# Kernel tuning notes

Measured on AMD Instinct MI355X. Metric: run time of the kernel, lower is better.

The kernel has to match this reference:

```python
import jax, jax.numpy as jnp
import numpy as np

E = 8          # num_experts
TOP_K = 2      # router top-k
ALPHA = 1.702  # swigluoai alpha
LIMIT = 7.0    # swigluoai clamp limit


def setup_inputs() -> dict:
    key = jax.random.key(0)
    ks = jax.random.split(key, 7)
    B, S, H, I = 2, 1024, 1024, 1024
    s = 1.0 / np.sqrt(H)  # keep activations O(1), realistic init scale
    return {
        "x": jax.random.normal(ks[0], (B, S, H), jnp.float32),
        "router_weight": jax.random.normal(ks[1], (E, H), jnp.float32) * s,
        "router_bias": jax.random.normal(ks[2], (E,), jnp.float32) * 0.01,
        "w1": jax.random.normal(ks[3], (E, H, 2 * I), jnp.float32) * s,  # interleaved gate/up
        "w1_bias": jax.random.normal(ks[4], (E, 2 * I), jnp.float32) * 0.01,
        "w2": jax.random.normal(ks[5], (E, I, H), jnp.float32) * s,
        "w2_bias": jax.random.normal(ks[6], (E, H), jnp.float32) * 0.01,
    }


def _moe(x, router_weight, router_bias, w1, w1_bias, w2, w2_bias):
    B, S, H = x.shape
    xf = x.reshape(-1, H)                                   # [T, H]
    # ---- router: softmax over expert logits, then top-k ----
    logits = xf @ router_weight.T + router_bias             # [T, E]
    probs = jax.nn.softmax(logits, axis=-1)
    expert_weights, expert_ids = jax.lax.top_k(probs, TOP_K)  # [T, k]
    # combine weights scattered to dense [T, E] (no normalization: normalize_expert_weights=None)
    combine = jnp.sum(jax.nn.one_hot(expert_ids, E, dtype=xf.dtype)
                      * expert_weights[..., None], axis=1)  # [T, E]
    # ---- grouped MLP, expressed densely per expert (reference semantics) ----
    h = jnp.einsum('th,ehi->eti', xf, w1) + w1_bias[:, None, :]   # [E, T, 2I]
    gate = h[..., 0::2]                                          # interleaved layout
    up = h[..., 1::2]
    gate = jnp.minimum(gate, LIMIT)                              # swigluoai: clamp gate max
    up = jnp.clip(up, -LIMIT, LIMIT)                             # clamp up both sides
    glu = gate * jax.nn.sigmoid(gate * ALPHA)
    act = (up + 1.0) * glu                                       # [E, T, I]
    y = jnp.einsum('eti,eih->eth', act, w2) + w2_bias[:, None, :]  # [E, T, H]
    out = jnp.einsum('eth,te->th', y, combine)                   # weighted combine
    return out.reshape(B, S, H), expert_weights


def reference(x, router_weight, router_bias, w1, w1_bias, w2, w2_bias):
    return _moe(x, router_weight, router_bias, w1, w1_bias, w2, w2_bias)
```

## Files before the change

### kernel.cpp

```cpp
#include <hip/hip_runtime.h>
#include <cstdint>
#include <cstddef>

typedef unsigned short u16;
typedef short bf16x8 __attribute__((ext_vector_type(8)));
typedef float floatx4 __attribute__((ext_vector_type(4)));

#define GLD16(gp, sp) __builtin_amdgcn_global_load_lds(                      \
    (const __attribute__((address_space(1))) void*)(gp),                     \
    (__attribute__((address_space(3))) void*)(sp), 16, 0, 0)

#define VWAIT(N) asm volatile("s_waitcnt vmcnt(" #N ")" ::: "memory")
#define BARF()                                                               \
  do {                                                                       \
    __builtin_amdgcn_sched_barrier(0);                                       \
    __builtin_amdgcn_s_barrier();                                            \
    __builtin_amdgcn_sched_barrier(0);                                       \
  } while (0)

__device__ __forceinline__ u16 f2bf(float f) {
  unsigned u = __float_as_uint(f);
  u += 0x7fffu + ((u >> 16) & 1u);
  return (u16)(u >> 16);
}

__device__ __forceinline__ void transpose64(const float* __restrict__ inb, u16* __restrict__ outb,
                                            int C, int r0, int c0) {
  __shared__ float tileT[64][65];
  const int t = threadIdx.x;
  const int k = t & 15, w = t >> 4;
#pragma unroll
  for (int it = 0; it < 4; ++it) {
    const int r = r0 + w + it * 16;
    const float4 v = *(const float4*)(inb + (size_t)r * C + (c0 + k * 4));
    tileT[k * 4 + 0][w + it * 16] = v.x;
    tileT[k * 4 + 1][w + it * 16] = v.y;
    tileT[k * 4 + 2][w + it * 16] = v.z;
    tileT[k * 4 + 3][w + it * 16] = v.w;
  }
  __syncthreads();
#pragma unroll
  for (int it = 0; it < 4; ++it) {
    const int cc = w + it * 16;
    const int r4 = k * 4;
    ushort4 o;
    o.x = f2bf(tileT[cc][r4 + 0]);
    o.y = f2bf(tileT[cc][r4 + 1]);
    o.z = f2bf(tileT[cc][r4 + 2]);
    o.w = f2bf(tileT[cc][r4 + 3]);
    *(ushort4*)(outb + (size_t)(c0 + cc) * 1024 + r0 + r4) = o;
  }
}

__global__ __launch_bounds__(256) void front_kernel(
    const float* __restrict__ x, const float* __restrict__ rw, const float* __restrict__ rb,
    float* __restrict__ ew, int* __restrict__ eids, float* __restrict__ eprobs,
    u16* __restrict__ xb,
    const float* __restrict__ w1, u16* __restrict__ w1t,
    const float* __restrict__ w2, u16* __restrict__ w2t) {
  const int bid = blockIdx.x;
  if (bid >= 512) {
    int idx = bid - 512;
    if (idx < 4096) {
      const int e = idx >> 9, rem = idx & 511;
      const int ct = rem & 31, rt = rem >> 5;
      transpose64(w1 + (size_t)e * 1024 * 2048, w1t + (size_t)e * 2048 * 1024,
                  2048, rt * 64, ct * 64);
    } else {
      idx -= 4096;
      const int e = idx >> 8, rem = idx & 255;
      const int ct = rem & 15, rt = rem >> 4;
      transpose64(w2 + (size_t)e * 1024 * 1024, w2t + (size_t)e * 1024 * 1024,
                  1024, rt * 64, ct * 64);
    }
    return;
  }
  const int wave = threadIdx.x >> 6, lane = threadIdx.x & 63;
  const int t = bid * 4 + wave;
  const float4* xv = (const float4*)(x + (size_t)t * 1024);
  ushort4* xo = (ushort4*)(xb + (size_t)t * 1024);
  float acc[8];
#pragma unroll
  for (int e = 0; e < 8; ++e) acc[e] = 0.f;
  for (int j = lane; j < 256; j += 64) {
    float4 xx = xv[j];
    ushort4 o;
    o.x = f2bf(xx.x); o.y = f2bf(xx.y); o.z = f2bf(xx.z); o.w = f2bf(xx.w);
    xo[j] = o;
#pragma unroll
    for (int e = 0; e < 8; ++e) {
      float4 wv = ((const float4*)(rw + (size_t)e * 1024))[j];
      acc[e] += xx.x * wv.x + xx.y * wv.y + xx.z * wv.z + xx.w * wv.w;
    }
  }
#pragma unroll
  for (int e = 0; e < 8; ++e) {
    float v = acc[e];
#pragma unroll
    for (int off = 32; off > 0; off >>= 1) v += __shfl_down(v, off);
    acc[e] = v;
  }
  if (lane == 0) {
    float p[8];
    float mx = -1e30f;
#pragma unroll
    for (int e = 0; e < 8; ++e) { p[e] = acc[e] + rb[e]; mx = fmaxf(mx, p[e]); }
    float sum = 0.f;
#pragma unroll
    for (int e = 0; e < 8; ++e) { p[e] = __expf(p[e] - mx); sum += p[e]; }
    float inv = 1.f / sum;
#pragma unroll
    for (int e = 0; e < 8; ++e) p[e] *= inv;
    int i0 = 0;
#pragma unroll
    for (int e = 1; e < 8; ++e) if (p[e] > p[i0]) i0 = e;
    int i1 = (i0 == 0) ? 1 : 0;
#pragma unroll
    for (int e = 0; e < 8; ++e) if (e != i0 && e != i1 && p[e] > p[i1]) i1 = e;
    ew[t * 2 + 0] = p[i0];
    ew[t * 2 + 1] = p[i1];
    eids[t * 2 + 0] = i0;
    eids[t * 2 + 1] = i1;
    eprobs[t * 2 + 0] = p[i0];
    eprobs[t * 2 + 1] = p[i1];
  }
}

__global__ void build_lists_kernel(const int* __restrict__ eids, const float* __restrict__ eprobs,
                                   int* __restrict__ row_token, float* __restrict__ row_scale,
                                   int* __restrict__ tok2slot, int* __restrict__ meta) {
  __shared__ int cnt[8], base[8], cur[8];
  const int tid = threadIdx.x;
  if (tid < 8) { cnt[tid] = 0; cur[tid] = 0; }
  __syncthreads();
  for (int t = tid; t < 2048; t += 256) {
    atomicAdd(&cnt[eids[t * 2 + 0]], 1);
    atomicAdd(&cnt[eids[t * 2 + 1]], 1);
  }
  __syncthreads();
  if (tid == 0) {
    int off = 0, w = 0;
    for (int e = 0; e < 8; ++e) {
      base[e] = off;
      meta[48 + e] = off;
      int nb = (cnt[e] + 127) >> 7;
      for (int rb = 0; rb < nb; ++rb) meta[1 + w++] = (e << 8) | rb;
      off += nb << 7;
    }
    meta[0] = w;
  }
  __syncthreads();
  for (int s = tid; s < 5120; s += 256) { row_token[s] = -1; row_scale[s] = 0.f; }
  __syncthreads();
  for (int t = tid; t < 2048; t += 256) {
#pragma unroll
    for (int k = 0; k < 2; ++k) {
      int e = eids[t * 2 + k];
      int s = base[e] + atomicAdd(&cur[e], 1);
      row_token[s] = t;
      row_scale[s] = eprobs[t * 2 + k];
      tok2slot[t * 2 + k] = s;
    }
  }
}

__device__ __forceinline__ void g1_compute(const u16* AsR, const u16* BsR, int wr, int wc,
                                           int lane, floatx4 (&acc)[4][4]) {
  bf16x8 af[4], bfr[4];
#pragma unroll
  for (int mi = 0; mi < 4; ++mi) af[mi] = *(const bf16x8*)(AsR + (wr * 4 + mi) * 512 + lane * 8);
#pragma unroll
  for (int ni = 0; ni < 4; ++ni) bfr[ni] = *(const bf16x8*)(BsR + (wc * 4 + ni) * 512 + lane * 8);
  __builtin_amdgcn_s_setprio(1);
#pragma unroll
  for (int mi = 0; mi < 4; ++mi)
#pragma unroll
    for (int ni = 0; ni < 4; ++ni)
      acc[mi][ni] = __builtin_amdgcn_mfma_f32_16x16x32_bf16(af[mi], bfr[ni], acc[mi][ni], 0, 0, 0);
  __builtin_amdgcn_s_setprio(0);
}

__global__ __launch_bounds__(256) void gemm1_act_kernel(
    const u16* __restrict__ xb, const u16* __restrict__ w1t,
    const float* __restrict__ w1b,
    const int* __restrict__ row_token, const float* __restrict__ row_scale,
    const int* __restrict__ meta, u16* __restrict__ actS) {
  if ((int)blockIdx.x >= meta[0]) return;
  __shared__ __align__(16) u16 As[3][128 * 32];
  __shared__ __align__(16) u16 Bs[3][128 * 32];
  const int w = meta[1 + blockIdx.x];
  const int e = w >> 8, rb = w & 255;
  const int slotB = meta[48 + e] + rb * 128;
  const int colBase = blockIdx.y * 128;
  const int tid = threadIdx.x, lane = tid & 63, wave = tid >> 6;
  const int row16 = lane & 15, chunk = lane >> 4;
  const u16* Bt = w1t + (size_t)e * 2048 * 1024;
  const u16* aP[2]; const u16* bP[2];
#pragma unroll
  for (int r = 0; r < 2; ++r) {
    int g = r * 4 + wave;
    int tk = row_token[slotB + g * 16 + row16];
    if (tk < 0) tk = 0;
    aP[r] = xb + (size_t)tk * 1024 + chunk * 8;
    bP[r] = Bt + (size_t)(colBase + g * 16 + row16) * 1024 + chunk * 8;
  }
  const int wr = wave >> 1, wc = wave & 1;
  floatx4 acc[4][4];
#pragma unroll
  for (int mi = 0; mi < 4; ++mi)
#pragma unroll
    for (int ni = 0; ni < 4; ++ni) acc[mi][ni] = floatx4{0.f, 0.f, 0.f, 0.f};

#define G1_STAGE(W, KT)                                                      \
  {                                                                          \
    const int kk = (KT) * 32;                                                \
    GLD16(aP[0] + kk, As[W] + wave * 512);                                   \
    GLD16(bP[0] + kk, Bs[W] + wave * 512);                                   \
    GLD16(aP[1] + kk, As[W] + (4 + wave) * 512);                             \
    GLD16(bP[1] + kk, Bs[W] + (4 + wave) * 512);                             \
  }

  G1_STAGE(0, 0);
  G1_STAGE(1, 1);

#pragma unroll 1
  for (int kt = 0; kt < 30; kt += 3) {
    G1_STAGE(2, kt + 2); VWAIT(8); BARF();
    g1_compute(As[0], Bs[0], wr, wc, lane, acc); BARF();
    G1_STAGE(0, kt + 3); VWAIT(8); BARF();
    g1_compute(As[1], Bs[1], wr, wc, lane, acc); BARF();
    G1_STAGE(1, kt + 4); VWAIT(8); BARF();
    g1_compute(As[2], Bs[2], wr, wc, lane, acc); BARF();
  }
  VWAIT(4); BARF();
  g1_compute(As[0], Bs[0], wr, wc, lane, acc); BARF();
  VWAIT(0); BARF();
  g1_compute(As[1], Bs[1], wr, wc, lane, acc);
#undef G1_STAGE

  const int cl = lane & 15, ql = lane >> 4;
#pragma unroll
  for (int mi = 0; mi < 4; ++mi) {
#pragma unroll
    for (int r = 0; r < 4; ++r) {
      const int slot = slotB + wr * 64 + mi * 16 + ql * 4 + r;
      const float c = row_scale[slot];
#pragma unroll
      for (int ni = 0; ni < 4; ++ni) {
        const int n = colBase + wc * 64 + ni * 16 + cl;
        float v = acc[mi][ni][r] + w1b[e * 2048 + n];
        float o = __shfl_xor(v, 1);
        if ((lane & 1) == 0) {
          float g = fminf(v, 7.f);
          float u = fminf(fmaxf(o, -7.f), 7.f);
          float sg = 1.f / (1.f + __expf(-1.702f * g));
          float a = (u + 1.f) * (g * sg);
          actS[(size_t)slot * 1024 + (n >> 1)] = f2bf(c * a);
        }
      }
    }
  }
}

__global__ __launch_bounds__(256) void gemm2_kernel(
    const u16* __restrict__ actS, const u16* __restrict__ w2t,
    const int* __restrict__ meta, float* __restrict__ y) {
  if ((int)blockIdx.x >= meta[0]) return;
  __shared__ __align__(16) u16 As[3][128 * 32];
  __shared__ __align__(16) u16 Bs[3][128 * 32];
  const int w = meta[1 + blockIdx.x];
  const int e = w >> 8, rb = w & 255;
  const int slotB = meta[48 + e] + rb * 128;
  const int colBase = blockIdx.y * 128;
  const int tid = threadIdx.x, lane = tid & 63, wave = tid >> 6;
  const int row16 = lane & 15, chunk = lane >> 4;
  const u16* Bt = w2t + (size_t)e * 1024 * 1024;
  const u16* aP[2]; const u16* bP[2];
#pragma unroll
  for (int r = 0; r < 2; ++r) {
    int g = r * 4 + wave;
    aP[r] = actS + (size_t)(slotB + g * 16 + row16) * 1024 + chunk * 8;
    bP[r] = Bt + (size_t)(colBase + g * 16 + row16) * 1024 + chunk * 8;
  }
  const int wr = wave >> 1, wc = wave & 1;
  floatx4 acc[4][4];
#pragma unroll
  for (int mi = 0; mi < 4; ++mi)
#pragma unroll
    for (int ni = 0; ni < 4; ++ni) acc[mi][ni] = floatx4{0.f, 0.f, 0.f, 0.f};

#define G2_STAGE(W, KT)                                                      \
  {                                                                          \
    const int kk = (KT) * 32;                                                \
    GLD16(aP[0] + kk, As[W] + wave * 512);                                   \
    GLD16(bP[0] + kk, Bs[W] + wave * 512);                                   \
    GLD16(aP[1] + kk, As[W] + (4 + wave) * 512);                             \
    GLD16(bP[1] + kk, Bs[W] + (4 + wave) * 512);                             \
  }

  G2_STAGE(0, 0);
  G2_STAGE(1, 1);

#pragma unroll 1
  for (int kt = 0; kt < 30; kt += 3) {
    G2_STAGE(2, kt + 2); VWAIT(8); BARF();
    g1_compute(As[0], Bs[0], wr, wc, lane, acc); BARF();
    G2_STAGE(0, kt + 3); VWAIT(8); BARF();
    g1_compute(As[1], Bs[1], wr, wc, lane, acc); BARF();
    G2_STAGE(1, kt + 4); VWAIT(8); BARF();
    g1_compute(As[2], Bs[2], wr, wc, lane, acc); BARF();
  }
  VWAIT(4); BARF();
  g1_compute(As[0], Bs[0], wr, wc, lane, acc); BARF();
  VWAIT(0); BARF();
  g1_compute(As[1], Bs[1], wr, wc, lane, acc);
#undef G2_STAGE

  const int cl = lane & 15, ql = lane >> 4;
#pragma unroll
  for (int mi = 0; mi < 4; ++mi)
#pragma unroll
    for (int r = 0; r < 4; ++r) {
      const int slot = slotB + wr * 64 + mi * 16 + ql * 4 + r;
#pragma unroll
      for (int ni = 0; ni < 4; ++ni) {
        const int col = colBase + wc * 64 + ni * 16 + cl;
        y[(size_t)slot * 1024 + col] = acc[mi][ni][r];
      }
    }
}

__global__ void combine_kernel(const float* __restrict__ y, const int* __restrict__ eids,
                               const float* __restrict__ eprobs, const int* __restrict__ tok2slot,
                               const float* __restrict__ w2b, float* __restrict__ out) {
  int idx = blockIdx.x * 256 + threadIdx.x;
  int t = idx >> 10, h = idx & 1023;
  int e0 = eids[t * 2], e1 = eids[t * 2 + 1];
  int s0 = tok2slot[t * 2], s1 = tok2slot[t * 2 + 1];
  out[idx] = eprobs[t * 2] * w2b[e0 * 1024 + h] + eprobs[t * 2 + 1] * w2b[e1 * 1024 + h]
           + y[(size_t)s0 * 1024 + h] + y[(size_t)s1 * 1024 + h];
}

extern "C" void kernel_launch(void* const* d_in, const int* in_sizes, int n_in,
                              void* d_out, int out_size, void* d_ws, size_t ws_size,
                              hipStream_t stream) {
  const float* x   = (const float*)d_in[0];
  const float* rw  = (const float*)d_in[1];
  const float* rb  = (const float*)d_in[2];
  const float* w1  = (const float*)d_in[3];
  const float* w1b = (const float*)d_in[4];
  const float* w2  = (const float*)d_in[5];
  const float* w2b = (const float*)d_in[6];
  float* out = (float*)d_out;
  float* ew  = out + (size_t)2048 * 1024;

  char* ws = (char*)d_ws;
  u16* xb        = (u16*)(ws);
  u16* w1t       = (u16*)(ws + (4ull << 20));
  float* y       = (float*)(ws + (4ull << 20));
  u16* w2t       = (u16*)(ws + (36ull << 20));
  u16* actS      = (u16*)(ws + (52ull << 20));
  int* eids      = (int*)(ws + (62ull << 20));
  float* eprobs  = (float*)(ws + (62ull << 20) + (16 << 10));
  int* row_token = (int*)(ws + (62ull << 20) + (32 << 10));
  float* row_scale = (float*)(ws + (62ull << 20) + (52 << 10));
  int* meta      = (int*)(ws + (62ull << 20) + (72 << 10));
  int* tok2slot  = (int*)(ws + (62ull << 20) + (74 << 10));

  front_kernel<<<512 + 4096 + 2048, 256, 0, stream>>>(x, rw, rb, ew, eids, eprobs, xb,
                                                      w1, w1t, w2, w2t);
  build_lists_kernel<<<1, 256, 0, stream>>>(eids, eprobs, row_token, row_scale, tok2slot, meta);
  gemm1_act_kernel<<<dim3(40, 16), 256, 0, stream>>>(xb, w1t, w1b, row_token, row_scale, meta, actS);
  gemm2_kernel<<<dim3(40, 8), 256, 0, stream>>>(actS, w2t, meta, y);
  combine_kernel<<<8192, 256, 0, stream>>>(y, eids, eprobs, tok2slot, w2b, out);
}
```

Before: 250.5 us.

## Fuse combine into gemm2 via atomic scatter-add and init output in gemm1

Removes the separate combine kernel and the intermediate y buffer. gemm1 blocks now also write the bias-weighted initial output (probability-weighted w2 bias), and gemm2 atomically adds its scaled results straight into the token rows of the output. This avoids writing and re-reading a 5120x1024 fp32 buffer and saves one launch. In exchange it adds float atomics, whose summation order is nondeterministic, and relies on gemm1 finishing before gemm2 on the same stream.

```diff
diff --git a/kernel.cpp b/kernel.cpp
--- a/kernel.cpp
+++ b/kernel.cpp
@@ -128,7 +128,7 @@
 
 __global__ void build_lists_kernel(const int* __restrict__ eids, const float* __restrict__ eprobs,
                                    int* __restrict__ row_token, float* __restrict__ row_scale,
-                                   int* __restrict__ tok2slot, int* __restrict__ meta) {
+                                   int* __restrict__ meta) {
   __shared__ int cnt[8], base[8], cur[8];
   const int tid = threadIdx.x;
   if (tid < 8) { cnt[tid] = 0; cur[tid] = 0; }
@@ -159,7 +159,6 @@
       int s = base[e] + atomicAdd(&cur[e], 1);
       row_token[s] = t;
       row_scale[s] = eprobs[t * 2 + k];
-      tok2slot[t * 2 + k] = s;
     }
   }
 }
@@ -184,7 +183,28 @@
     const u16* __restrict__ xb, const u16* __restrict__ w1t,
     const float* __restrict__ w1b,
     const int* __restrict__ row_token, const float* __restrict__ row_scale,
-    const int* __restrict__ meta, u16* __restrict__ actS) {
+    const int* __restrict__ meta, u16* __restrict__ actS,
+    const int* __restrict__ eids, const float* __restrict__ eprobs,
+    const float* __restrict__ w2b, float* __restrict__ out) {
+  const int tid = threadIdx.x;
+  {
+    const int gtid = (blockIdx.y * gridDim.x + blockIdx.x) * 256 + tid;
+    const float4* b4 = (const float4*)w2b;
+    float4* o4 = (float4*)out;
+    for (int i = gtid; i < 524288; i += 640 * 256) {
+      const int t = i >> 8, h4 = i & 255;
+      const int e0 = eids[t * 2], e1 = eids[t * 2 + 1];
+      const float p0 = eprobs[t * 2], p1 = eprobs[t * 2 + 1];
+      const float4 b0 = b4[e0 * 256 + h4];
+      const float4 b1 = b4[e1 * 256 + h4];
+      float4 r;
+      r.x = p0 * b0.x + p1 * b1.x;
+      r.y = p0 * b0.y + p1 * b1.y;
+      r.z = p0 * b0.z + p1 * b1.z;
+      r.w = p0 * b0.w + p1 * b1.w;
+      o4[i] = r;
+    }
+  }
   if ((int)blockIdx.x >= meta[0]) return;
   __shared__ __align__(16) u16 As[3][128 * 32];
   __shared__ __align__(16) u16 Bs[3][128 * 32];
@@ -192,7 +212,7 @@
   const int e = w >> 8, rb = w & 255;
   const int slotB = meta[48 + e] + rb * 128;
   const int colBase = blockIdx.y * 128;
-  const int tid = threadIdx.x, lane = tid & 63, wave = tid >> 6;
+  const int lane = tid & 63, wave = tid >> 6;
   const int row16 = lane & 15, chunk = lane >> 4;
   const u16* Bt = w1t + (size_t)e * 2048 * 1024;
   const u16* aP[2]; const u16* bP[2];
@@ -264,7 +284,8 @@
 
 __global__ __launch_bounds__(256) void gemm2_kernel(
     const u16* __restrict__ actS, const u16* __restrict__ w2t,
-    const int* __restrict__ meta, float* __restrict__ y) {
+    const int* __restrict__ row_token, const int* __restrict__ meta,
+    float* __restrict__ out) {
   if ((int)blockIdx.x >= meta[0]) return;
   __shared__ __align__(16) u16 As[3][128 * 32];
   __shared__ __align__(16) u16 Bs[3][128 * 32];
@@ -322,23 +343,14 @@
 #pragma unroll
     for (int r = 0; r < 4; ++r) {
       const int slot = slotB + wr * 64 + mi * 16 + ql * 4 + r;
+      const int tok = row_token[slot];
+      if (tok < 0) continue;
 #pragma unroll
       for (int ni = 0; ni < 4; ++ni) {
         const int col = colBase + wc * 64 + ni * 16 + cl;
-        y[(size_t)slot * 1024 + col] = acc[mi][ni][r];
+        atomicAdd(out + (size_t)tok * 1024 + col, acc[mi][ni][r]);
       }
     }
-}
-
-__global__ void combine_kernel(const float* __restrict__ y, const int* __restrict__ eids,
-                               const float* __restrict__ eprobs, const int* __restrict__ tok2slot,
-                               const float* __restrict__ w2b, float* __restrict__ out) {
-  int idx = blockIdx.x * 256 + threadIdx.x;
-  int t = idx >> 10, h = idx & 1023;
-  int e0 = eids[t * 2], e1 = eids[t * 2 + 1];
-  int s0 = tok2slot[t * 2], s1 = tok2slot[t * 2 + 1];
-  out[idx] = eprobs[t * 2] * w2b[e0 * 1024 + h] + eprobs[t * 2 + 1] * w2b[e1 * 1024 + h]
-           + y[(size_t)s0 * 1024 + h] + y[(size_t)s1 * 1024 + h];
 }
 
 extern "C" void kernel_launch(void* const* d_in, const int* in_sizes, int n_in,
@@ -357,7 +369,6 @@
   char* ws = (char*)d_ws;
   u16* xb        = (u16*)(ws);
   u16* w1t       = (u16*)(ws + (4ull << 20));
-  float* y       = (float*)(ws + (4ull << 20));
   u16* w2t       = (u16*)(ws + (36ull << 20));
   u16* actS      = (u16*)(ws + (52ull << 20));
   int* eids      = (int*)(ws + (62ull << 20));
@@ -365,12 +376,11 @@
   int* row_token = (int*)(ws + (62ull << 20) + (32 << 10));
   float* row_scale = (float*)(ws + (62ull << 20) + (52 << 10));
   int* meta      = (int*)(ws + (62ull << 20) + (72 << 10));
-  int* tok2slot  = (int*)(ws + (62ull << 20) + (74 << 10));
 
   front_kernel<<<512 + 4096 + 2048, 256, 0, stream>>>(x, rw, rb, ew, eids, eprobs, xb,
                                                       w1, w1t, w2, w2t);
-  build_lists_kernel<<<1, 256, 0, stream>>>(eids, eprobs, row_token, row_scale, tok2slot, meta);
-  gemm1_act_kernel<<<dim3(40, 16), 256, 0, stream>>>(xb, w1t, w1b, row_token, row_scale, meta, actS);
-  gemm2_kernel<<<dim3(40, 8), 256, 0, stream>>>(actS, w2t, meta, y);
-  combine_kernel<<<8192, 256, 0, stream>>>(y, eids, eprobs, tok2slot, w2b, out);
-}
+  build_lists_kernel<<<1, 256, 0, stream>>>(eids, eprobs, row_token, row_scale, meta);
+  gemm1_act_kernel<<<dim3(40, 16), 256, 0, stream>>>(xb, w1t, w1b, row_token, row_scale,
+                                                     meta, actS, eids, eprobs, w2b, out);
+  gemm2_kernel<<<dim3(40, 8), 256, 0, stream>>>(actS, w2t, row_token, meta, out);
+}
```

After: 254.0 us. No clear change (+1.4%).
